# Optimization experiments

Measured on AMD Instinct MI355X. Metric: run time of the kernel, lower is better.

## Reference

```python
import jax, jax.numpy as jnp
import numpy as np

B, S, DIN, DOUT = 4, 4096, 4096, 4096
W_SCALE = 0.02  # kaiming-ish scale; keeps values inside fp8 range


def setup_inputs() -> dict:
    key = jax.random.key(0)
    k1, k2, k3 = jax.random.split(key, 3)
    x = jax.random.normal(k1, (B, S, DIN), dtype=jnp.float16)
    weight = (jax.random.normal(k2, (DOUT, DIN), dtype=jnp.float32) * W_SCALE).astype(jnp.float16)
    bias = (jax.random.normal(k3, (DOUT,), dtype=jnp.float32) * W_SCALE).astype(jnp.float16)
    return {"x": x, "weight": weight, "bias": bias}


def reference(x, weight, bias):
    # Emulate torch._scaled_mm: activations quantized to fp8 e5m2,
    # weight (transposed) quantized to fp8 e4m3fn, scale_a = scale_b = 1.0,
    # accumulate in fp32, add fp16 bias, output fp16.
    out_shape = x.shape[:-1] + (weight.shape[0],)
    x8 = x.reshape(-1, x.shape[-1]).astype(jnp.float8_e5m2)       # [M, DIN]
    w8 = weight.T.astype(jnp.float8_e4m3fn)                        # [DIN, DOUT]
    scale = jnp.float32(1.0)  # scale_a * scale_b
    acc = jnp.matmul(x8.astype(jnp.float32), w8.astype(jnp.float32))  # [M, DOUT] fp32 accum
    out = (acc * scale + bias.astype(jnp.float32)).astype(jnp.float16)
    return out.reshape(out_shape)
```

## Files before the change

### kernel.cpp

```cpp
#include <hip/hip_runtime.h>
#include <hip/hip_fp16.h>

#define M_DIM 16384
#define N_DIM 4096
#define K_DIM 4096

typedef __attribute__((ext_vector_type(16))) float f32x16;
typedef __attribute__((ext_vector_type(4)))  int   i32x4;
typedef __attribute__((ext_vector_type(8)))  int   i32x8;

union frag_u { i32x8 v; i32x4 h[2]; };

__global__ __launch_bounds__(256) void quant_fused_kernel(
    const float* __restrict__ x, const float* __restrict__ w,
    uint4* __restrict__ xq, uint4* __restrict__ wq)
{
  const int b = blockIdx.x;
  const float* in;
  uint4* out;
  int t;
  bool e4m3;
  if (b < 16384) { in = x; out = xq; t = b * 256 + threadIdx.x; e4m3 = false; }
  else { in = w; out = wq; t = (b - 16384) * 256 + threadIdx.x; e4m3 = true; }

  const int g    = t & 1023;
  const int tile = t >> 10;
  const int kt   = tile & 63;
  const int bt   = tile >> 6;
  const int sb   = g >> 7;
  const int half = (g >> 6) & 1;
  const int l    = g & 63;
  const int row  = bt * 256 + sb * 32 + (l & 31);
  const int k    = kt * 64 + (l >> 5) * 32 + half * 16;

  const float4* p = reinterpret_cast<const float4*>(in + (size_t)row * K_DIM + k);
  float4 v0 = p[0], v1 = p[1], v2 = p[2], v3 = p[3];
  int w0 = 0, w1 = 0, w2 = 0, w3 = 0;
  if (e4m3) {
    w0 = __builtin_amdgcn_cvt_pk_fp8_f32(v0.x, v0.y, w0, false);
    w0 = __builtin_amdgcn_cvt_pk_fp8_f32(v0.z, v0.w, w0, true);
    w1 = __builtin_amdgcn_cvt_pk_fp8_f32(v1.x, v1.y, w1, false);
    w1 = __builtin_amdgcn_cvt_pk_fp8_f32(v1.z, v1.w, w1, true);
    w2 = __builtin_amdgcn_cvt_pk_fp8_f32(v2.x, v2.y, w2, false);
    w2 = __builtin_amdgcn_cvt_pk_fp8_f32(v2.z, v2.w, w2, true);
    w3 = __builtin_amdgcn_cvt_pk_fp8_f32(v3.x, v3.y, w3, false);
    w3 = __builtin_amdgcn_cvt_pk_fp8_f32(v3.z, v3.w, w3, true);
  } else {
    w0 = __builtin_amdgcn_cvt_pk_bf8_f32(v0.x, v0.y, w0, false);
    w0 = __builtin_amdgcn_cvt_pk_bf8_f32(v0.z, v0.w, w0, true);
    w1 = __builtin_amdgcn_cvt_pk_bf8_f32(v1.x, v1.y, w1, false);
    w1 = __builtin_amdgcn_cvt_pk_bf8_f32(v1.z, v1.w, w1, true);
    w2 = __builtin_amdgcn_cvt_pk_bf8_f32(v2.x, v2.y, w2, false);
    w2 = __builtin_amdgcn_cvt_pk_bf8_f32(v2.z, v2.w, w2, true);
    w3 = __builtin_amdgcn_cvt_pk_bf8_f32(v3.x, v3.y, w3, false);
    w3 = __builtin_amdgcn_cvt_pk_bf8_f32(v3.z, v3.w, w3, true);
  }
  out[t] = make_uint4((unsigned)w0, (unsigned)w1, (unsigned)w2, (unsigned)w3);
}

__global__ __launch_bounds__(512, 2) void gemm_fp8_kernel(
    const unsigned char* __restrict__ Aq,
    const unsigned char* __restrict__ Wq,
    const float* __restrict__ bias,
    float* __restrict__ C)
{
  __shared__ __align__(16) unsigned char lds[131072];

  const int tid  = threadIdx.x;
  const int lane = tid & 63;
  const int wave = tid >> 6;
  const int wr   = wave >> 2;
  const int wc   = wave & 3;

  const int bid = blockIdx.x;
  const int swz = (bid & 7) * 128 + (bid >> 3);
  const int bmi = swz >> 4;
  const int bni = swz & 15;

  const unsigned char* tA = Aq + (size_t)bmi * (64 * 16384);
  const unsigned char* tB = Wq + (size_t)bni * (64 * 16384);

  const size_t t16 = (size_t)tid * 16;
  const int    w1k = wave * 1024;

#define STAGE(gb, lo_)                                                      \
  __builtin_amdgcn_global_load_lds(                                        \
      (const __attribute__((address_space(1))) void*)((gb) + t16),          \
      (__attribute__((address_space(3))) void*)(lds + (lo_) + w1k), 16, 0, 0)

#define STAGE_TILE(tp, base)                                                \
  STAGE(tA + (tp), (base));          STAGE(tA + (tp) + 8192, (base) + 8192); \
  STAGE(tB + (tp), (base) + 16384);  STAGE(tB + (tp) + 8192, (base) + 24576)

#define RD8(dst, off)                                                       \
  { const unsigned char* _p = lds + (off) + lane * 16;                      \
    (dst).h[0] = *reinterpret_cast<const i32x4*>(_p);                       \
    (dst).h[1] = *reinterpret_cast<const i32x4*>(_p + 1024); }

#define MFMA(d, a, b)                                                       \
  d = __builtin_amdgcn_mfma_scale_f32_32x32x64_f8f6f4(                      \
      a, b, d, 1 , 0 , 0, 0x7F7F7F7F, 0, 0x7F7F7F7F)

#define SBAR __builtin_amdgcn_sched_barrier(0)
#define P1   __builtin_amdgcn_s_setprio(1)
#define P0   __builtin_amdgcn_s_setprio(0)

  const int aoff = wr * 8192;
  const int boff = 16384 + wc * 4096;

  f32x16 acc[4][2] = {};
  frag_u Ea0, Ea1, Ea2, Ea3, Eb0, Eb1;
  frag_u Oa0, Oa1, Oa2, Oa3, Ob0, Ob1;

#define RDTILE(s, buf)                                                      \
  RD8(s##a0, (buf) + aoff);        RD8(s##a1, (buf) + aoff + 2048);         \
  RD8(s##a2, (buf) + aoff + 4096); RD8(s##a3, (buf) + aoff + 6144);         \
  RD8(s##b0, (buf) + boff);        RD8(s##b1, (buf) + boff + 2048)

#define MFMAC(s)                                                            \
  P1;                                                                       \
  MFMA(acc[0][0], s##a0.v, s##b0.v);  MFMA(acc[0][1], s##a0.v, s##b1.v);    \
  MFMA(acc[1][0], s##a1.v, s##b0.v);  MFMA(acc[1][1], s##a1.v, s##b1.v);    \
  MFMA(acc[2][0], s##a2.v, s##b0.v);  MFMA(acc[2][1], s##a2.v, s##b1.v);    \
  MFMA(acc[3][0], s##a3.v, s##b0.v);  MFMA(acc[3][1], s##a3.v, s##b1.v);    \
  P0

#define TAIL(stbuf, tp)                                                     \
  SBAR;                                                                     \
  STAGE_TILE(tp, stbuf);                                                    \
  SBAR;                                                                     \
  asm volatile("s_waitcnt vmcnt(4)" ::: "memory");                          \
  SBAR;                                                                     \
  __builtin_amdgcn_s_barrier()

#define TILE_RF(rdset, mfset, rdbuf, stbuf, tp)                             \
  SBAR; RDTILE(rdset, rdbuf); SBAR; MFMAC(mfset); TAIL(stbuf, tp)
#define TILE_FR(rdset, mfset, rdbuf, stbuf, tp)                             \
  SBAR; MFMAC(mfset); SBAR; RDTILE(rdset, rdbuf); TAIL(stbuf, tp)

  STAGE_TILE(0, 0);
  STAGE_TILE(16384, 32768);
  STAGE_TILE(32768, 65536);
  SBAR;
  asm volatile("s_waitcnt vmcnt(4)" ::: "memory");
  SBAR;
  __builtin_amdgcn_s_barrier();
  SBAR;
  RDTILE(E, 0);
  SBAR;

  if (wr == 0) {
    for (int it = 0; it < 16; ++it) {
      const int t = it << 2;
      const size_t tp3 = (size_t)((t + 3) & 63) * 16384;
      const size_t tp4 = (size_t)((t + 4) & 63) * 16384;
      const size_t tp5 = (size_t)((t + 5) & 63) * 16384;
      const size_t tp6 = (size_t)((t + 6) & 63) * 16384;
      TILE_RF(O, E, 32768, 98304, tp3);
      TILE_RF(E, O, 65536, 0,     tp4);
      TILE_RF(O, E, 98304, 32768, tp5);
      TILE_RF(E, O, 0,     65536, tp6);
    }
  } else {
    for (int it = 0; it < 16; ++it) {
      const int t = it << 2;
      const size_t tp3 = (size_t)((t + 3) & 63) * 16384;
      const size_t tp4 = (size_t)((t + 4) & 63) * 16384;
      const size_t tp5 = (size_t)((t + 5) & 63) * 16384;
      const size_t tp6 = (size_t)((t + 6) & 63) * 16384;
      TILE_FR(O, E, 32768, 98304, tp3);
      TILE_FR(E, O, 65536, 0,     tp4);
      TILE_FR(O, E, 98304, 32768, tp5);
      TILE_FR(E, O, 0,     65536, tp6);
    }
  }
#undef STAGE
#undef STAGE_TILE
#undef RD8
#undef RDTILE
#undef MFMA
#undef MFMAC
#undef TAIL
#undef TILE_RF
#undef TILE_FR
#undef SBAR
#undef P1
#undef P0

  #pragma unroll
  for (int n = 0; n < 2; ++n) {
    const int col = bni * 256 + wc * 64 + n * 32 + (lane & 31);
    const float bv = bias[col];
    #pragma unroll
    for (int m = 0; m < 4; ++m) {
      const int rbase = bmi * 256 + wr * 128 + m * 32 + ((lane >> 5) << 2);
      #pragma unroll
      for (int r = 0; r < 16; ++r) {
        const int row = rbase + (r & 3) + 8 * (r >> 2);
        C[(size_t)row * N_DIM + col] =
            __half2float(__float2half_rn(acc[m][n][r] + bv));
      }
    }
  }
}

extern "C" void kernel_launch(void* const* d_in, const int* in_sizes, int n_in,
                              void* d_out, int out_size, void* d_ws, size_t ws_size,
                              hipStream_t stream) {
  const float* x  = (const float*)d_in[0];
  const float* w  = (const float*)d_in[1];
  const float* bs = (const float*)d_in[2];
  float* out = (float*)d_out;

  unsigned char* xq = (unsigned char*)d_ws;
  unsigned char* wq = (unsigned char*)d_ws + (size_t)M_DIM * K_DIM;

  quant_fused_kernel<<<20480, 256, 0, stream>>>(x, w, (uint4*)xq, (uint4*)wq);

  gemm_fp8_kernel<<<1024, 512, 0, stream>>>(xq, wq, bs, out);
}
```

Before: 347.7 us.

## Shrink GEMM block tile to 128x128 with 4 waves and simpler pipeline

Changes the GEMM tile from 256x256 with 8 waves to 128x128 with 4 waves. Each wave now holds a 2x2 set of 32x32 accumulators instead of 4x2, LDS per block drops to 64KB, and the grid grows to 4096 blocks. The quantization kernel's packed layout is changed to match the 128-row tiles. The wave-specialized read/MFMA ordering is replaced by a single uniform schedule. Smaller tiles lower the arithmetic intensity and double the global traffic per FLOP, in exchange for more blocks and possibly higher occupancy.

```diff
diff --git a/kernel.cpp b/kernel.cpp
--- a/kernel.cpp
+++ b/kernel.cpp
@@ -23,14 +23,14 @@
   if (b < 16384) { in = x; out = xq; t = b * 256 + threadIdx.x; e4m3 = false; }
   else { in = w; out = wq; t = (b - 16384) * 256 + threadIdx.x; e4m3 = true; }
 
-  const int g    = t & 1023;
-  const int tile = t >> 10;
+  const int g    = t & 511;
+  const int tile = t >> 9;
   const int kt   = tile & 63;
   const int bt   = tile >> 6;
   const int sb   = g >> 7;
   const int half = (g >> 6) & 1;
   const int l    = g & 63;
-  const int row  = bt * 256 + sb * 32 + (l & 31);
+  const int row  = bt * 128 + sb * 32 + (l & 31);
   const int k    = kt * 64 + (l >> 5) * 32 + half * 16;
 
   const float4* p = reinterpret_cast<const float4*>(in + (size_t)row * K_DIM + k);
@@ -58,27 +58,27 @@
   out[t] = make_uint4((unsigned)w0, (unsigned)w1, (unsigned)w2, (unsigned)w3);
 }
 
-__global__ __launch_bounds__(512, 2) void gemm_fp8_kernel(
+__global__ __launch_bounds__(256, 2) void gemm_fp8_kernel(
     const unsigned char* __restrict__ Aq,
     const unsigned char* __restrict__ Wq,
     const float* __restrict__ bias,
     float* __restrict__ C)
 {
-  __shared__ __align__(16) unsigned char lds[131072];
+  __shared__ __align__(16) unsigned char lds[65536];
 
   const int tid  = threadIdx.x;
   const int lane = tid & 63;
   const int wave = tid >> 6;
-  const int wr   = wave >> 2;
-  const int wc   = wave & 3;
+  const int wr   = wave >> 1;
+  const int wc   = wave & 1;
 
   const int bid = blockIdx.x;
-  const int swz = (bid & 7) * 128 + (bid >> 3);
-  const int bmi = swz >> 4;
-  const int bni = swz & 15;
-
-  const unsigned char* tA = Aq + (size_t)bmi * (64 * 16384);
-  const unsigned char* tB = Wq + (size_t)bni * (64 * 16384);
+  const int swz = (bid & 7) * 512 + (bid >> 3);
+  const int bni = swz >> 7;
+  const int bmi = swz & 127;
+
+  const unsigned char* tA = Aq + (size_t)bmi * (64 * 8192);
+  const unsigned char* tB = Wq + (size_t)bni * (64 * 8192);
 
   const size_t t16 = (size_t)tid * 16;
   const int    w1k = wave * 1024;
@@ -89,8 +89,8 @@
       (__attribute__((address_space(3))) void*)(lds + (lo_) + w1k), 16, 0, 0)
 
 #define STAGE_TILE(tp, base)                                                \
-  STAGE(tA + (tp), (base));          STAGE(tA + (tp) + 8192, (base) + 8192); \
-  STAGE(tB + (tp), (base) + 16384);  STAGE(tB + (tp) + 8192, (base) + 24576)
+  STAGE(tA + (tp), (base));          STAGE(tA + (tp) + 4096, (base) + 4096); \
+  STAGE(tB + (tp), (base) + 8192);   STAGE(tB + (tp) + 4096, (base) + 12288)
 
 #define RD8(dst, off)                                                       \
   { const unsigned char* _p = lds + (off) + lane * 16;                      \
@@ -105,27 +105,28 @@
 #define P1   __builtin_amdgcn_s_setprio(1)
 #define P0   __builtin_amdgcn_s_setprio(0)
 
-  const int aoff = wr * 8192;
-  const int boff = 16384 + wc * 4096;
-
-  f32x16 acc[4][2] = {};
-  frag_u Ea0, Ea1, Ea2, Ea3, Eb0, Eb1;
-  frag_u Oa0, Oa1, Oa2, Oa3, Ob0, Ob1;
+  const int aoff = wr * 4096;
+  const int boff = 8192 + wc * 4096;
+
+  f32x16 acc[2][2] = {};
+  frag_u Ea0, Ea1, Eb0, Eb1;
+  frag_u Oa0, Oa1, Ob0, Ob1;
 
 #define RDTILE(s, buf)                                                      \
-  RD8(s##a0, (buf) + aoff);        RD8(s##a1, (buf) + aoff + 2048);         \
-  RD8(s##a2, (buf) + aoff + 4096); RD8(s##a3, (buf) + aoff + 6144);         \
-  RD8(s##b0, (buf) + boff);        RD8(s##b1, (buf) + boff + 2048)
+  RD8(s##a0, (buf) + aoff); RD8(s##a1, (buf) + aoff + 2048);                \
+  RD8(s##b0, (buf) + boff); RD8(s##b1, (buf) + boff + 2048)
 
 #define MFMAC(s)                                                            \
   P1;                                                                       \
   MFMA(acc[0][0], s##a0.v, s##b0.v);  MFMA(acc[0][1], s##a0.v, s##b1.v);    \
   MFMA(acc[1][0], s##a1.v, s##b0.v);  MFMA(acc[1][1], s##a1.v, s##b1.v);    \
-  MFMA(acc[2][0], s##a2.v, s##b0.v);  MFMA(acc[2][1], s##a2.v, s##b1.v);    \
-  MFMA(acc[3][0], s##a3.v, s##b0.v);  MFMA(acc[3][1], s##a3.v, s##b1.v);    \
   P0
 
-#define TAIL(stbuf, tp)                                                     \
+#define TILE_STEP(rdset, mfset, rdbuf, stbuf, tp)                           \
+  SBAR;                                                                     \
+  RDTILE(rdset, rdbuf);                                                     \
+  SBAR;                                                                     \
+  MFMAC(mfset);                                                             \
   SBAR;                                                                     \
   STAGE_TILE(tp, stbuf);                                                    \
   SBAR;                                                                     \
@@ -133,14 +134,9 @@
   SBAR;                                                                     \
   __builtin_amdgcn_s_barrier()
 
-#define TILE_RF(rdset, mfset, rdbuf, stbuf, tp)                             \
-  SBAR; RDTILE(rdset, rdbuf); SBAR; MFMAC(mfset); TAIL(stbuf, tp)
-#define TILE_FR(rdset, mfset, rdbuf, stbuf, tp)                             \
-  SBAR; MFMAC(mfset); SBAR; RDTILE(rdset, rdbuf); TAIL(stbuf, tp)
-
   STAGE_TILE(0, 0);
+  STAGE_TILE(8192, 16384);
   STAGE_TILE(16384, 32768);
-  STAGE_TILE(32768, 65536);
   SBAR;
   asm volatile("s_waitcnt vmcnt(4)" ::: "memory");
   SBAR;
@@ -149,30 +145,16 @@
   RDTILE(E, 0);
   SBAR;
 
-  if (wr == 0) {
-    for (int it = 0; it < 16; ++it) {
-      const int t = it << 2;
-      const size_t tp3 = (size_t)((t + 3) & 63) * 16384;
-      const size_t tp4 = (size_t)((t + 4) & 63) * 16384;
-      const size_t tp5 = (size_t)((t + 5) & 63) * 16384;
-      const size_t tp6 = (size_t)((t + 6) & 63) * 16384;
-      TILE_RF(O, E, 32768, 98304, tp3);
-      TILE_RF(E, O, 65536, 0,     tp4);
-      TILE_RF(O, E, 98304, 32768, tp5);
-      TILE_RF(E, O, 0,     65536, tp6);
-    }
-  } else {
-    for (int it = 0; it < 16; ++it) {
-      const int t = it << 2;
-      const size_t tp3 = (size_t)((t + 3) & 63) * 16384;
-      const size_t tp4 = (size_t)((t + 4) & 63) * 16384;
-      const size_t tp5 = (size_t)((t + 5) & 63) * 16384;
-      const size_t tp6 = (size_t)((t + 6) & 63) * 16384;
-      TILE_FR(O, E, 32768, 98304, tp3);
-      TILE_FR(E, O, 65536, 0,     tp4);
-      TILE_FR(O, E, 98304, 32768, tp5);
-      TILE_FR(E, O, 0,     65536, tp6);
-    }
+  for (int it = 0; it < 16; ++it) {
+    const int t = it << 2;
+    const size_t tp3 = (size_t)((t + 3) & 63) * 8192;
+    const size_t tp4 = (size_t)((t + 4) & 63) * 8192;
+    const size_t tp5 = (size_t)((t + 5) & 63) * 8192;
+    const size_t tp6 = (size_t)((t + 6) & 63) * 8192;
+    TILE_STEP(O, E, 16384, 49152, tp3);
+    TILE_STEP(E, O, 32768, 0,     tp4);
+    TILE_STEP(O, E, 49152, 16384, tp5);
+    TILE_STEP(E, O, 0,     32768, tp6);
   }
 #undef STAGE
 #undef STAGE_TILE
@@ -180,20 +162,18 @@
 #undef RDTILE
 #undef MFMA
 #undef MFMAC
-#undef TAIL
-#undef TILE_RF
-#undef TILE_FR
+#undef TILE_STEP
 #undef SBAR
 #undef P1
 #undef P0
 
   #pragma unroll
   for (int n = 0; n < 2; ++n) {
-    const int col = bni * 256 + wc * 64 + n * 32 + (lane & 31);
+    const int col = bni * 128 + wc * 64 + n * 32 + (lane & 31);
     const float bv = bias[col];
     #pragma unroll
-    for (int m = 0; m < 4; ++m) {
-      const int rbase = bmi * 256 + wr * 128 + m * 32 + ((lane >> 5) << 2);
+    for (int m = 0; m < 2; ++m) {
+      const int rbase = bmi * 128 + wr * 64 + m * 32 + ((lane >> 5) << 2);
       #pragma unroll
       for (int r = 0; r < 16; ++r) {
         const int row = rbase + (r & 3) + 8 * (r >> 2);
@@ -217,5 +197,5 @@
 
   quant_fused_kernel<<<20480, 256, 0, stream>>>(x, w, (uint4*)xq, (uint4*)wq);
 
-  gemm_fp8_kernel<<<1024, 512, 0, stream>>>(xq, wq, bs, out);
+  gemm_fp8_kernel<<<4096, 256, 0, stream>>>(xq, wq, bs, out);
 }
```

After: 440.0 us. 26.5% more time.

## Coalesce quantization reads by staging packed FP8 tiles through LDS

Applied to the files above, without the earlier changes.

The quant kernel now has each block handle one full 256x64 tile. Four threads cover a contiguous 256-byte row segment, so fp32 reads are coalesced, whereas before each lane read a different row in the MFMA-packed order. Converted fp8 values are written into a swizzled LDS buffer in the packed layout, then written out to global memory contiguously. This adds an LDS round trip and a __syncthreads, and cuts the grid to a quarter as many blocks with four times the work per thread.

```diff
diff --git a/kernel.cpp b/kernel.cpp
--- a/kernel.cpp
+++ b/kernel.cpp
@@ -15,47 +15,58 @@
     const float* __restrict__ x, const float* __restrict__ w,
     uint4* __restrict__ xq, uint4* __restrict__ wq)
 {
+  __shared__ __align__(16) unsigned char sts[16384];
   const int b = blockIdx.x;
   const float* in;
   uint4* out;
-  int t;
+  int tile;
   bool e4m3;
-  if (b < 16384) { in = x; out = xq; t = b * 256 + threadIdx.x; e4m3 = false; }
-  else { in = w; out = wq; t = (b - 16384) * 256 + threadIdx.x; e4m3 = true; }
-
-  const int g    = t & 1023;
-  const int tile = t >> 10;
-  const int kt   = tile & 63;
-  const int bt   = tile >> 6;
-  const int sb   = g >> 7;
-  const int half = (g >> 6) & 1;
-  const int l    = g & 63;
-  const int row  = bt * 256 + sb * 32 + (l & 31);
-  const int k    = kt * 64 + (l >> 5) * 32 + half * 16;
-
-  const float4* p = reinterpret_cast<const float4*>(in + (size_t)row * K_DIM + k);
-  float4 v0 = p[0], v1 = p[1], v2 = p[2], v3 = p[3];
-  int w0 = 0, w1 = 0, w2 = 0, w3 = 0;
-  if (e4m3) {
-    w0 = __builtin_amdgcn_cvt_pk_fp8_f32(v0.x, v0.y, w0, false);
-    w0 = __builtin_amdgcn_cvt_pk_fp8_f32(v0.z, v0.w, w0, true);
-    w1 = __builtin_amdgcn_cvt_pk_fp8_f32(v1.x, v1.y, w1, false);
-    w1 = __builtin_amdgcn_cvt_pk_fp8_f32(v1.z, v1.w, w1, true);
-    w2 = __builtin_amdgcn_cvt_pk_fp8_f32(v2.x, v2.y, w2, false);
-    w2 = __builtin_amdgcn_cvt_pk_fp8_f32(v2.z, v2.w, w2, true);
-    w3 = __builtin_amdgcn_cvt_pk_fp8_f32(v3.x, v3.y, w3, false);
-    w3 = __builtin_amdgcn_cvt_pk_fp8_f32(v3.z, v3.w, w3, true);
-  } else {
-    w0 = __builtin_amdgcn_cvt_pk_bf8_f32(v0.x, v0.y, w0, false);
-    w0 = __builtin_amdgcn_cvt_pk_bf8_f32(v0.z, v0.w, w0, true);
-    w1 = __builtin_amdgcn_cvt_pk_bf8_f32(v1.x, v1.y, w1, false);
-    w1 = __builtin_amdgcn_cvt_pk_bf8_f32(v1.z, v1.w, w1, true);
-    w2 = __builtin_amdgcn_cvt_pk_bf8_f32(v2.x, v2.y, w2, false);
-    w2 = __builtin_amdgcn_cvt_pk_bf8_f32(v2.z, v2.w, w2, true);
-    w3 = __builtin_amdgcn_cvt_pk_bf8_f32(v3.x, v3.y, w3, false);
-    w3 = __builtin_amdgcn_cvt_pk_bf8_f32(v3.z, v3.w, w3, true);
-  }
-  out[t] = make_uint4((unsigned)w0, (unsigned)w1, (unsigned)w2, (unsigned)w3);
+  if (b < 4096) { in = x; out = xq; tile = b; e4m3 = false; }
+  else          { in = w; out = wq; tile = b - 4096; e4m3 = true; }
+  const int kt = tile & 63;
+  const int bt = tile >> 6;
+  const int t  = threadIdx.x;
+
+  #pragma unroll
+  for (int iter = 0; iter < 4; ++iter) {
+    const int r = iter * 64 + (t >> 2);
+    const int c = t & 3;
+    const float4* p = reinterpret_cast<const float4*>(
+        in + (size_t)(bt * 256 + r) * K_DIM + kt * 64 + c * 16);
+    float4 v0 = p[0], v1 = p[1], v2 = p[2], v3 = p[3];
+    int w0 = 0, w1 = 0, w2 = 0, w3 = 0;
+    if (e4m3) {
+      w0 = __builtin_amdgcn_cvt_pk_fp8_f32(v0.x, v0.y, w0, false);
+      w0 = __builtin_amdgcn_cvt_pk_fp8_f32(v0.z, v0.w, w0, true);
+      w1 = __builtin_amdgcn_cvt_pk_fp8_f32(v1.x, v1.y, w1, false);
+      w1 = __builtin_amdgcn_cvt_pk_fp8_f32(v1.z, v1.w, w1, true);
+      w2 = __builtin_amdgcn_cvt_pk_fp8_f32(v2.x, v2.y, w2, false);
+      w2 = __builtin_amdgcn_cvt_pk_fp8_f32(v2.z, v2.w, w2, true);
+      w3 = __builtin_amdgcn_cvt_pk_fp8_f32(v3.x, v3.y, w3, false);
+      w3 = __builtin_amdgcn_cvt_pk_fp8_f32(v3.z, v3.w, w3, true);
+    } else {
+      w0 = __builtin_amdgcn_cvt_pk_bf8_f32(v0.x, v0.y, w0, false);
+      w0 = __builtin_amdgcn_cvt_pk_bf8_f32(v0.z, v0.w, w0, true);
+      w1 = __builtin_amdgcn_cvt_pk_bf8_f32(v1.x, v1.y, w1, false);
+      w1 = __builtin_amdgcn_cvt_pk_bf8_f32(v1.z, v1.w, w1, true);
+      w2 = __builtin_amdgcn_cvt_pk_bf8_f32(v2.x, v2.y, w2, false);
+      w2 = __builtin_amdgcn_cvt_pk_bf8_f32(v2.z, v2.w, w2, true);
+      w3 = __builtin_amdgcn_cvt_pk_bf8_f32(v3.x, v3.y, w3, false);
+      w3 = __builtin_amdgcn_cvt_pk_bf8_f32(v3.z, v3.w, w3, true);
+    }
+    int ppos = (r >> 5) * 2048 + (c & 1) * 1024 + (c >> 1) * 512 + (r & 31) * 16;
+    ppos ^= ((ppos >> 9) & 3) << 4;
+    *reinterpret_cast<uint4*>(sts + ppos) = make_uint4(
+        (unsigned)w0, (unsigned)w1, (unsigned)w2, (unsigned)w3);
+  }
+  __syncthreads();
+  const size_t obase = (size_t)tile * 1024;
+  #pragma unroll
+  for (int j = 0; j < 4; ++j) {
+    const int q  = j * 4096 + t * 16;
+    const int qs = q ^ (((q >> 9) & 3) << 4);
+    out[obase + (q >> 4)] = *reinterpret_cast<const uint4*>(sts + qs);
+  }
 }
 
 __global__ __launch_bounds__(512, 2) void gemm_fp8_kernel(
@@ -215,7 +226,7 @@
   unsigned char* xq = (unsigned char*)d_ws;
   unsigned char* wq = (unsigned char*)d_ws + (size_t)M_DIM * K_DIM;
 
-  quant_fused_kernel<<<20480, 256, 0, stream>>>(x, w, (uint4*)xq, (uint4*)wq);
+  quant_fused_kernel<<<5120, 256, 0, stream>>>(x, w, (uint4*)xq, (uint4*)wq);
 
   gemm_fp8_kernel<<<1024, 512, 0, stream>>>(xq, wq, bs, out);
 }
```

Result: no change. 342.4 us, median of 2 (-1.5%).
